# Optimization experiments

Hardware: AMD Instinct MI355X
Metric: run time of the kernel (lower is better)

Reference implementation:

```python
import jax, jax.numpy as jnp
import numpy as np
import math

N_LAYERS = 6
F = 512   # num_feature
H = 8     # num_head
DH = F // H
V = 32000 # vocab size
B = 64
S = 512   # == PositionalEncoding max_len
EPS = 1e-5


def _make_pe(max_len, d_model):
    position = np.arange(max_len, dtype=np.float32)[:, None]
    div_term = np.exp(np.arange(0, d_model, 2, dtype=np.float32) * (-math.log(10000.0) / d_model))
    pe = np.zeros((max_len, d_model), dtype=np.float32)
    pe[:, 0::2] = np.sin(position * div_term)
    pe[:, 1::2] = np.cos(position * div_term)
    return jnp.asarray(pe)


def setup_inputs() -> dict:
    key = jax.random.key(0)
    ks = jax.random.split(key, 16)
    w = lambda k, shape, s=0.02: (jax.random.normal(k, shape, dtype=jnp.float32) * s)
    inp = {
        "text": jax.random.randint(ks[0], (B, S), 0, V),
        "emb": jax.random.normal(ks[1], (V, F), dtype=jnp.float32) * 0.25,
        "pe": _make_pe(S, F),
        # per-layer params stacked on leading N axis
        "Wq": w(ks[2], (N_LAYERS, F, F)), "bq": jnp.zeros((N_LAYERS, F), jnp.float32),
        "Wk": w(ks[3], (N_LAYERS, F, F)), "bk": jnp.zeros((N_LAYERS, F), jnp.float32),
        "Wv": w(ks[4], (N_LAYERS, F, F)), "bv": jnp.zeros((N_LAYERS, F), jnp.float32),
        "g1": jnp.ones((N_LAYERS, F), jnp.float32), "beta1": jnp.zeros((N_LAYERS, F), jnp.float32),
        "Wf": w(ks[5], (N_LAYERS, F, F)), "bf": jnp.zeros((N_LAYERS, F), jnp.float32),
        "g2": jnp.ones((N_LAYERS, F), jnp.float32), "beta2": jnp.zeros((N_LAYERS, F), jnp.float32),
    }
    return inp


def _layernorm(x, g, b):
    m = jnp.mean(x, axis=-1, keepdims=True)
    v = jnp.mean(jnp.square(x - m), axis=-1, keepdims=True)
    return (x - m) * jax.lax.rsqrt(v + EPS) * g + b


def _encoder_layer(x, Wq, bq, Wk, bk, Wv, bv, g1, beta1, Wf, bf, g2, beta2):
    Bz, Sz, Fz = x.shape
    q = (x @ Wq + bq).reshape(Bz, Sz, H, DH)
    k = (x @ Wk + bk).reshape(Bz, Sz, H, DH)
    v = (x @ Wv + bv).reshape(Bz, Sz, H, DH)
    # FAITHFUL to source bug: attention over HEADS per token, no 1/sqrt(d) scaling.
    score = jnp.einsum('bshd,bsgd->bshg', q, k)          # [B,S,H,H]
    weight = jax.nn.softmax(score, axis=-1)
    attn = jnp.einsum('bshg,bsgd->bshd', weight, v).reshape(Bz, Sz, Fz)
    x = _layernorm(attn + x, g1, beta1)
    x = _layernorm((x @ Wf + bf) + x, g2, beta2)
    return x


def reference(text, emb, pe, Wq, bq, Wk, bk, Wv, bv, g1, beta1, Wf, bf, g2, beta2):
    x = emb[text] + pe[None, :text.shape[1], :]  # embedding + pos-enc (dropout = eval identity)
    for i in range(N_LAYERS):
        x = _encoder_layer(x, Wq[i], bq[i], Wk[i], bk[i], Wv[i], bv[i],
                           g1[i], beta1[i], Wf[i], bf[i], g2[i], beta2[i])
    return x
```

## Files before the change

kernel.cpp:

```cpp
#include <hip/hip_runtime.h>
#include <stdint.h>

typedef unsigned short u16;
using frag8 = __attribute__((ext_vector_type(8))) short;
using f32x4 = __attribute__((ext_vector_type(4))) float;

#define NTOK 32768
#define FDIM 512

__device__ __forceinline__ float bflo(uint32_t p){ union{uint32_t u; float f;} v; v.u = p<<16; return v.f; }
__device__ __forceinline__ float bfhi(uint32_t p){ union{uint32_t u; float f;} v; v.u = p & 0xffff0000u; return v.f; }
__device__ __forceinline__ float bf1(u16 x){ union{uint32_t u; float f;} v; v.u = ((uint32_t)x)<<16; return v.f; }
__device__ __forceinline__ u16 f2bf(float f){
  union{float f; uint32_t u;} v; v.f = f;
  uint32_t u = v.u;
  u += 0x7fffu + ((u>>16)&1u);
  return (u16)(u>>16);
}

__device__ __forceinline__ void async16(const void* g, void* l){
  __builtin_amdgcn_global_load_lds((const __attribute__((address_space(1))) uint32_t*)g,
                                   (__attribute__((address_space(3))) uint32_t*)l, 16, 0, 0);
}

__global__ __launch_bounds__(256) void embed_kernel(const int* __restrict__ text,
    const float* __restrict__ emb, const float* __restrict__ pe,
    u16* __restrict__ xb, const int tok0){
  const int gid = blockIdx.x*256 + threadIdx.x;
  const int base = gid*4;
  const int tl = base >> 9;
  const int f  = base & 511;
  const int tg = tl + tok0;
  const int s  = tg & 511;
  const int tok = text[tg];
  const float4 e4 = *(const float4*)(emb + (size_t)tok*FDIM + f);
  const float4 p4 = *(const float4*)(pe  + (size_t)s*FDIM + f);
  ushort4 ob;
  ob.x = f2bf(e4.x + p4.x);
  ob.y = f2bf(e4.y + p4.y);
  ob.z = f2bf(e4.z + p4.z);
  ob.w = f2bf(e4.w + p4.w);
  *(ushort4*)(xb + base) = ob;
}

__global__ __launch_bounds__(256) void transpose_w(const float* __restrict__ Wq,
    const float* __restrict__ Wk, const float* __restrict__ Wv, const float* __restrict__ Wf,
    u16* __restrict__ WT){
  const int gid = blockIdx.x*256 + threadIdx.x;
  const int n   = gid & 2047;
  const int k8  = (gid>>11) & 63;
  const int lay = gid >> 17;
  const float* src; int col;
  if      (n <  512){ src = Wq; col = n;      }
  else if (n < 1024){ src = Wk; col = n-512;  }
  else if (n < 1536){ src = Wv; col = n-1024; }
  else              { src = Wf; col = n-1536; }
  src += (size_t)lay*FDIM*FDIM;
  u16 vals[8] __attribute__((aligned(16)));
  #pragma unroll
  for (int i=0;i<8;i++) vals[i] = f2bf(src[(size_t)(k8*8+i)*FDIM + col]);
  *(int4*)(WT + ((size_t)lay*2048 + n)*FDIM + k8*8) = *(const int4*)vals;
}

template<int MODE>
__global__ __launch_bounds__(512, 2) void gemm256(
    const u16* __restrict__ A, const u16* __restrict__ BT,
    const float* __restrict__ b0, const float* __restrict__ b1, const float* __restrict__ b2,
    const u16* __restrict__ resid, u16* __restrict__ C, const int ldC, const int NB){
  __shared__ __attribute__((aligned(16))) short As[4*256*32];
  __shared__ __attribute__((aligned(16))) short Bs[4*256*32];
  const int nwg = gridDim.x;
  const int orig = blockIdx.x;
  const int wg = ((nwg & 7) == 0) ? ((orig & 7)*(nwg >> 3) + (orig >> 3)) : orig;
  const int nblk = wg % NB, mblk = wg / NB;
  const int m0 = mblk << 8, n0 = nblk << 8;
  const int tid = threadIdx.x;
  const int wid = tid >> 6, l = tid & 63;
  const int lm = l & 15, quad = l >> 4;

  const int srow = wid*16 + (l >> 2);
  const int sch  = (l & 3) ^ ((l >> 3) & 3);
  const char* Asrc0 = (const char*)A  + ((size_t)(m0 + srow))*1024 + sch*16;
  const char* Asrc1 = Asrc0 + 128*1024;
  const char* Bsrc0 = (const char*)BT + ((size_t)(n0 + srow))*1024 + sch*16;
  const char* Bsrc1 = Bsrc0 + 128*1024;
  char* ldsAw = (char*)As + wid*1024;
  char* ldsBw = (char*)Bs + wid*1024;

  f32x4 acc[8][4];
  #pragma unroll
  for (int i=0;i<8;i++)
    #pragma unroll
    for (int j=0;j<4;j++){ f32x4 z = {0.f,0.f,0.f,0.f}; acc[i][j] = z; }

  const int rsel = quad ^ ((lm >> 1) & 3);
  const int aB = ((wid>>2)*128 + lm)*32 + rsel*8;
  const int bB = ((wid&3)*64  + lm)*32 + rsel*8;

  #pragma unroll
  for (int kt=0; kt<3; kt++){
    async16(Asrc0 + kt*64, ldsAw + kt*16384);
    async16(Asrc1 + kt*64, ldsAw + kt*16384 + 8192);
    async16(Bsrc0 + kt*64, ldsBw + kt*16384);
    async16(Bsrc1 + kt*64, ldsBw + kt*16384 + 8192);
  }

  for (int t=0; t<16; ++t){
    if (t < 14)       asm volatile("s_waitcnt vmcnt(8)" ::: "memory");
    else if (t == 14) asm volatile("s_waitcnt vmcnt(4)" ::: "memory");
    else              asm volatile("s_waitcnt vmcnt(0)" ::: "memory");
    __builtin_amdgcn_s_barrier();
    asm volatile("" ::: "memory");
    const int slot = t & 3;
    const short* sA = As + slot*8192;
    const short* sB = Bs + slot*8192;
    frag8 af[4], bf[4], ag[4];
    #pragma unroll
    for (int mi=0; mi<4; mi++) af[mi] = *(const frag8*)(sA + aB + mi*512);
    #pragma unroll
    for (int nj=0; nj<4; nj++) bf[nj] = *(const frag8*)(sB + bB + nj*512);
    if (t < 13){
      const int s3 = (t+3) & 3, off = (t+3)*64;
      async16(Asrc0 + off, ldsAw + s3*16384);
      async16(Asrc1 + off, ldsAw + s3*16384 + 8192);
    }
    __builtin_amdgcn_s_setprio(1);
    #pragma unroll
    for (int mi=0; mi<4; mi++)
      #pragma unroll
      for (int nj=0; nj<4; nj++)
        acc[mi][nj] = __builtin_amdgcn_mfma_f32_16x16x32_bf16(af[mi], bf[nj], acc[mi][nj], 0,0,0);
    __builtin_amdgcn_s_setprio(0);
    #pragma unroll
    for (int mi=0; mi<4; mi++) ag[mi] = *(const frag8*)(sA + aB + 2048 + mi*512);
    if (t < 13){
      const int s3 = (t+3) & 3, off = (t+3)*64;
      async16(Bsrc0 + off, ldsBw + s3*16384);
      async16(Bsrc1 + off, ldsBw + s3*16384 + 8192);
    }
    __builtin_amdgcn_s_setprio(1);
    #pragma unroll
    for (int mi=0; mi<4; mi++)
      #pragma unroll
      for (int nj=0; nj<4; nj++)
        acc[4+mi][nj] = __builtin_amdgcn_mfma_f32_16x16x32_bf16(ag[mi], bf[nj], acc[4+mi][nj], 0,0,0);
    __builtin_amdgcn_s_setprio(0);
  }

  float bias[4]; int cols[4];
  #pragma unroll
  for (int nj=0;nj<4;nj++){
    const int c = n0 + (wid&3)*64 + nj*16 + lm;
    cols[nj] = c;
    if (MODE==0) bias[nj] = (c<512 ? b0[c] : (c<1024 ? b1[c-512] : b2[c-1024]));
    else         bias[nj] = b0[c];
  }
  #pragma unroll
  for (int mi=0; mi<8; mi++){
    const int rbase = m0 + (wid>>2)*128 + mi*16 + quad*4;
    #pragma unroll
    for (int r=0;r<4;r++){
      const size_t row = (size_t)(rbase + r);
      #pragma unroll
      for (int nj=0;nj<4;nj++){
        float v = acc[mi][nj][r] + bias[nj];
        if (MODE==1) v += bf1(resid[row*FDIM + cols[nj]]);
        C[row*(size_t)ldC + cols[nj]] = f2bf(v);
      }
    }
  }
}

__global__ __launch_bounds__(256) void attn_ln1(const u16* __restrict__ qkvb,
    const u16* __restrict__ xb, const float* __restrict__ gam, const float* __restrict__ bet,
    u16* __restrict__ y1b){
  __shared__ __attribute__((aligned(16))) u16 sQ[4][1536];
  __shared__ float sWt[4][64];
  const int tid = threadIdx.x, w = tid>>6, l = tid&63;
  const int t = blockIdx.x*4 + w;
  {
    const int4* src = (const int4*)(qkvb + (size_t)t*1536);
    int4* dst = (int4*)(&sQ[w][0]);
    #pragma unroll
    for (int i=0;i<3;i++) dst[i*64 + l] = src[i*64 + l];
  }
  __syncthreads();
  const int h = l>>3, g = l&7;
  const u16* qrow = &sQ[w][h*64];
  const u16* krow = &sQ[w][512 + g*64];
  float sc = 0.f;
  const int dstart = (l&31)*2;
  #pragma unroll
  for (int i=0;i<32;i++){
    const int d = (dstart + 2*i) & 63;
    const uint32_t qp = *(const uint32_t*)(qrow + d);
    const uint32_t kp = *(const uint32_t*)(krow + d);
    sc += bflo(qp)*bflo(kp) + bfhi(qp)*bfhi(kp);
  }
  float mx = sc;
  mx = fmaxf(mx, __shfl_xor(mx,1));
  mx = fmaxf(mx, __shfl_xor(mx,2));
  mx = fmaxf(mx, __shfl_xor(mx,4));
  const float e = __expf(sc - mx);
  float ssum = e;
  ssum += __shfl_xor(ssum,1);
  ssum += __shfl_xor(ssum,2);
  ssum += __shfl_xor(ssum,4);
  sWt[w][l] = e / ssum;
  __syncthreads();
  float wt[8];
  #pragma unroll
  for (int gg=0;gg<8;gg++) wt[gg] = sWt[w][h*8+gg];
  float att[8] = {0,0,0,0,0,0,0,0};
  const int d0 = (l&7)*8;
  #pragma unroll
  for (int gg=0;gg<8;gg++){
    const int4 vv = *(const int4*)(&sQ[w][1024 + gg*64 + d0]);
    const uint32_t* vp = (const uint32_t*)&vv;
    #pragma unroll
    for (int p=0;p<4;p++){
      att[2*p]   += wt[gg]*bflo(vp[p]);
      att[2*p+1] += wt[gg]*bfhi(vp[p]);
    }
  }
  const size_t rb = (size_t)t*FDIM + l*8;
  const int4 xv = *(const int4*)(xb + rb);
  const uint32_t* xp = (const uint32_t*)&xv;
  float y[8]; float s1=0.f, s2=0.f;
  #pragma unroll
  for (int p=0;p<4;p++){
    y[2*p]   = att[2*p]   + bflo(xp[p]);
    y[2*p+1] = att[2*p+1] + bfhi(xp[p]);
  }
  #pragma unroll
  for (int j=0;j<8;j++){ s1 += y[j]; s2 += y[j]*y[j]; }
  #pragma unroll
  for (int off=1; off<64; off<<=1){ s1 += __shfl_xor(s1,off); s2 += __shfl_xor(s2,off); }
  const float mean = s1*(1.f/512.f);
  const float var  = s2*(1.f/512.f) - mean*mean;
  const float rstd = rsqrtf(var + 1e-5f);
  const float4 g0 = *(const float4*)(gam + l*8);
  const float4 g1v = *(const float4*)(gam + l*8 + 4);
  const float4 b0v = *(const float4*)(bet + l*8);
  const float4 b1v = *(const float4*)(bet + l*8 + 4);
  float of[8];
  of[0]=(y[0]-mean)*rstd*g0.x + b0v.x;
  of[1]=(y[1]-mean)*rstd*g0.y + b0v.y;
  of[2]=(y[2]-mean)*rstd*g0.z + b0v.z;
  of[3]=(y[3]-mean)*rstd*g0.w + b0v.w;
  of[4]=(y[4]-mean)*rstd*g1v.x + b1v.x;
  of[5]=(y[5]-mean)*rstd*g1v.y + b1v.y;
  of[6]=(y[6]-mean)*rstd*g1v.z + b1v.z;
  of[7]=(y[7]-mean)*rstd*g1v.w + b1v.w;
  u16 ob[8] __attribute__((aligned(16)));
  #pragma unroll
  for (int j=0;j<8;j++) ob[j] = f2bf(of[j]);
  *(int4*)(y1b + rb) = *(const int4*)ob;
}

__global__ __launch_bounds__(256) void ln2_kernel(const u16* __restrict__ z,
    const float* __restrict__ gam, const float* __restrict__ bet,
    u16* __restrict__ xb, float* __restrict__ outp, const int final_){
  const int tid = threadIdx.x, w = tid>>6, l = tid&63;
  const int t = blockIdx.x*4 + w;
  const size_t rb = (size_t)t*FDIM + l*8;
  const int4 zv = *(const int4*)(z + rb);
  const uint32_t* zp = (const uint32_t*)&zv;
  float y[8];
  #pragma unroll
  for (int p=0;p<4;p++){ y[2*p]=bflo(zp[p]); y[2*p+1]=bfhi(zp[p]); }
  float s1=0.f, s2=0.f;
  #pragma unroll
  for (int j=0;j<8;j++){ s1+=y[j]; s2+=y[j]*y[j]; }
  #pragma unroll
  for (int off=1; off<64; off<<=1){ s1 += __shfl_xor(s1,off); s2 += __shfl_xor(s2,off); }
  const float mean = s1*(1.f/512.f);
  const float var  = s2*(1.f/512.f) - mean*mean;
  const float rstd = rsqrtf(var + 1e-5f);
  const float4 g0 = *(const float4*)(gam + l*8);
  const float4 g1v = *(const float4*)(gam + l*8 + 4);
  const float4 b0v = *(const float4*)(bet + l*8);
  const float4 b1v = *(const float4*)(bet + l*8 + 4);
  float of[8];
  of[0]=(y[0]-mean)*rstd*g0.x + b0v.x;
  of[1]=(y[1]-mean)*rstd*g0.y + b0v.y;
  of[2]=(y[2]-mean)*rstd*g0.z + b0v.z;
  of[3]=(y[3]-mean)*rstd*g0.w + b0v.w;
  of[4]=(y[4]-mean)*rstd*g1v.x + b1v.x;
  of[5]=(y[5]-mean)*rstd*g1v.y + b1v.y;
  of[6]=(y[6]-mean)*rstd*g1v.z + b1v.z;
  of[7]=(y[7]-mean)*rstd*g1v.w + b1v.w;
  if (final_){
    float4 o0; o0.x=of[0]; o0.y=of[1]; o0.z=of[2]; o0.w=of[3];
    float4 o1; o1.x=of[4]; o1.y=of[5]; o1.z=of[6]; o1.w=of[7];
    *(float4*)(outp + rb) = o0;
    *(float4*)(outp + rb + 4) = o1;
  } else {
    u16 ob[8] __attribute__((aligned(16)));
    #pragma unroll
    for (int j=0;j<8;j++) ob[j] = f2bf(of[j]);
    *(int4*)(xb + rb) = *(const int4*)ob;
  }
}

extern "C" void kernel_launch(void* const* d_in, const int* in_sizes, int n_in,
                              void* d_out, int out_size, void* d_ws, size_t ws_size,
                              hipStream_t stream){
  const int*   text = (const int*)d_in[0];
  const float* emb = (const float*)d_in[1];
  const float* pe  = (const float*)d_in[2];
  const float* Wq  = (const float*)d_in[3];
  const float* bq  = (const float*)d_in[4];
  const float* Wk  = (const float*)d_in[5];
  const float* bk  = (const float*)d_in[6];
  const float* Wv  = (const float*)d_in[7];
  const float* bv  = (const float*)d_in[8];
  const float* g1  = (const float*)d_in[9];
  const float* be1 = (const float*)d_in[10];
  const float* Wf  = (const float*)d_in[11];
  const float* bf_ = (const float*)d_in[12];
  const float* g2  = (const float*)d_in[13];
  const float* be2 = (const float*)d_in[14];
  float* outp = (float*)d_out;

  const size_t wtB = (size_t)6*2048*512*2;
  int T = NTOK;
  while (T > 2048 && wtB + (size_t)T*5120 > ws_size) T >>= 1;

  char* ws = (char*)d_ws;
  u16*   WT  = (u16*)ws;
  char*  act = ws + wtB;
  u16*   xb  = (u16*)act;
  u16*   y1b = (u16*)(act + (size_t)T*1024);
  u16*   qkv = (u16*)(act + (size_t)T*2048);
  u16*   zb  = qkv;

  hipLaunchKernelGGL(transpose_w, dim3(3072), dim3(256), 0, stream, Wq, Wk, Wv, Wf, WT);

  const int chunks = NTOK / T;
  for (int c = 0; c < chunks; c++){
    const int tok0 = c*T;
    hipLaunchKernelGGL(embed_kernel, dim3(T/2), dim3(256), 0, stream, text, emb, pe, xb, tok0);
    for (int lay=0; lay<6; lay++){
      const u16* WTl = WT + (size_t)lay*2048*FDIM;
      hipLaunchKernelGGL((gemm256<0>), dim3((T/256)*6), dim3(512), 0, stream,
          xb, WTl, bq + lay*FDIM, bk + lay*FDIM, bv + lay*FDIM, (const u16*)nullptr, qkv, 1536, 6);
      hipLaunchKernelGGL(attn_ln1, dim3(T/4), dim3(256), 0, stream,
          qkv, xb, g1 + lay*FDIM, be1 + lay*FDIM, y1b);
      hipLaunchKernelGGL((gemm256<1>), dim3((T/256)*2), dim3(512), 0, stream,
          y1b, WTl + (size_t)1536*FDIM, bf_ + lay*FDIM, (const float*)nullptr, (const float*)nullptr,
          y1b, zb, 512, 2);
      hipLaunchKernelGGL(ln2_kernel, dim3(T/4), dim3(256), 0, stream,
          zb, g2 + lay*FDIM, be2 + lay*FDIM, xb, outp + (size_t)tok0*FDIM, (lay==5)?1:0);
    }
  }
}
```

Measured before the change: 969.0 us.

## Software-pipeline LDS fragment loads across K-tiles in GEMM main loop

Restructures the GEMM K-loop so the A and B fragments for the next tile are read from LDS while the second half of the current tile's MFMAs runs. B fragments are double-buffered in registers. The wait and barrier move mid-tile, with an extra barrier at the end of each step to protect slot reuse. The goal is to hide LDS read latency behind MFMA work, at the cost of more registers and an extra barrier per step.

```diff
diff --git a/kernel.cpp b/kernel.cpp
--- a/kernel.cpp
+++ b/kernel.cpp
@@ -104,48 +104,67 @@
     async16(Bsrc0 + kt*64, ldsBw + kt*16384);
     async16(Bsrc1 + kt*64, ldsBw + kt*16384 + 8192);
   }
-
-  for (int t=0; t<16; ++t){
-    if (t < 14)       asm volatile("s_waitcnt vmcnt(8)" ::: "memory");
-    else if (t == 14) asm volatile("s_waitcnt vmcnt(4)" ::: "memory");
-    else              asm volatile("s_waitcnt vmcnt(0)" ::: "memory");
-    __builtin_amdgcn_s_barrier();
-    asm volatile("" ::: "memory");
-    const int slot = t & 3;
-    const short* sA = As + slot*8192;
-    const short* sB = Bs + slot*8192;
-    frag8 af[4], bf[4], ag[4];
-    #pragma unroll
-    for (int mi=0; mi<4; mi++) af[mi] = *(const frag8*)(sA + aB + mi*512);
-    #pragma unroll
-    for (int nj=0; nj<4; nj++) bf[nj] = *(const frag8*)(sB + bB + nj*512);
-    if (t < 13){
-      const int s3 = (t+3) & 3, off = (t+3)*64;
-      async16(Asrc0 + off, ldsAw + s3*16384);
-      async16(Asrc1 + off, ldsAw + s3*16384 + 8192);
-    }
-    __builtin_amdgcn_s_setprio(1);
-    #pragma unroll
-    for (int mi=0; mi<4; mi++)
-      #pragma unroll
-      for (int nj=0; nj<4; nj++)
-        acc[mi][nj] = __builtin_amdgcn_mfma_f32_16x16x32_bf16(af[mi], bf[nj], acc[mi][nj], 0,0,0);
-    __builtin_amdgcn_s_setprio(0);
-    #pragma unroll
-    for (int mi=0; mi<4; mi++) ag[mi] = *(const frag8*)(sA + aB + 2048 + mi*512);
-    if (t < 13){
-      const int s3 = (t+3) & 3, off = (t+3)*64;
-      async16(Bsrc0 + off, ldsBw + s3*16384);
-      async16(Bsrc1 + off, ldsBw + s3*16384 + 8192);
-    }
-    __builtin_amdgcn_s_setprio(1);
-    #pragma unroll
-    for (int mi=0; mi<4; mi++)
-      #pragma unroll
-      for (int nj=0; nj<4; nj++)
-        acc[4+mi][nj] = __builtin_amdgcn_mfma_f32_16x16x32_bf16(ag[mi], bf[nj], acc[4+mi][nj], 0,0,0);
-    __builtin_amdgcn_s_setprio(0);
-  }
+  frag8 aC[4], aN[4], bE[4], bO[4];
+  asm volatile("s_waitcnt vmcnt(8)" ::: "memory");
+  __builtin_amdgcn_s_barrier();
+  #pragma unroll
+  for (int x=0;x<4;x++){
+    aC[x] = *(const frag8*)(As + aB + x*512);
+    bE[x] = *(const frag8*)(Bs + bB + x*512);
+  }
+
+#define MFMA16(AF, BF, RO) \
+  __builtin_amdgcn_s_setprio(1); \
+  _Pragma("unroll") \
+  for (int mi_=0; mi_<4; mi_++) \
+    _Pragma("unroll") \
+    for (int nj_=0; nj_<4; nj_++) \
+      acc[(RO)+mi_][nj_] = __builtin_amdgcn_mfma_f32_16x16x32_bf16(AF[mi_], BF[nj_], acc[(RO)+mi_][nj_], 0,0,0); \
+  __builtin_amdgcn_s_setprio(0);
+
+#define TILE_BODY(T_, BU, BL, DOSTAGE, VMC) { \
+  const short* sA_ = As + ((T_)&3)*8192; \
+  if (DOSTAGE){ \
+    const int s3_ = ((T_)+3)&3; const int off_ = ((T_)+3)*64; \
+    async16(Asrc0 + off_, ldsAw + s3_*16384); \
+    async16(Asrc1 + off_, ldsAw + s3_*16384 + 8192); \
+  } \
+  _Pragma("unroll") \
+  for (int x_=0;x_<4;x_++) aN[x_] = *(const frag8*)(sA_ + aB + 2048 + x_*512); \
+  MFMA16(aC, BU, 0) \
+  if (DOSTAGE){ \
+    const int s3_ = ((T_)+3)&3; const int off_ = ((T_)+3)*64; \
+    async16(Bsrc0 + off_, ldsBw + s3_*16384); \
+    async16(Bsrc1 + off_, ldsBw + s3_*16384 + 8192); \
+  } \
+  asm volatile("s_waitcnt vmcnt(" #VMC ")" ::: "memory"); \
+  __builtin_amdgcn_s_barrier(); \
+  { const short* sA2_ = As + (((T_)+1)&3)*8192; \
+    const short* sB2_ = Bs + (((T_)+1)&3)*8192; \
+    _Pragma("unroll") \
+    for (int x_=0;x_<4;x_++){ \
+      aC[x_] = *(const frag8*)(sA2_ + aB + x_*512); \
+      BL[x_] = *(const frag8*)(sB2_ + bB + x_*512); } } \
+  MFMA16(aN, BU, 4) \
+  __builtin_amdgcn_s_barrier(); \
+}
+
+  for (int tp=0; tp<6; ++tp){
+    TILE_BODY(2*tp,   bE, bO, 1, 8)
+    TILE_BODY(2*tp+1, bO, bE, 1, 8)
+  }
+  TILE_BODY(12, bE, bO, 1, 8)
+  TILE_BODY(13, bO, bE, 0, 4)
+  TILE_BODY(14, bE, bO, 0, 0)
+  {
+    const short* sA_ = As + 3*8192;
+    #pragma unroll
+    for (int x=0;x<4;x++) aN[x] = *(const frag8*)(sA_ + aB + 2048 + x*512);
+    MFMA16(aC, bO, 0)
+    MFMA16(aN, bO, 4)
+  }
+#undef TILE_BODY
+#undef MFMA16
 
   float bias[4]; int cols[4];
   #pragma unroll
```

Result: faster. 916.3 us (-5.4%).

## Shrink GEMM tiles to 128x128 with 4 waves and 3-stage LDS pipeline

Applied to the files above, without the earlier changes.

Replaces the 256x256-tile, 8-wave GEMM, which used a 4-slot LDS ring, with a 128x128-tile, 4-wave kernel that uses a 3-slot ring and a fully unrolled K loop. The grids grow by 4x, which improves load balance and occupancy (3 blocks per CU, less LDS per block). The cost is more global and L2 traffic per FLOP, since each tile reuses less data, and a shallower prefetch depth.

```diff
diff --git a/kernel.cpp b/kernel.cpp
--- a/kernel.cpp
+++ b/kernel.cpp
@@ -63,17 +63,17 @@
 }
 
 template<int MODE>
-__global__ __launch_bounds__(512, 2) void gemm256(
+__global__ __launch_bounds__(256, 3) void gemm128(
     const u16* __restrict__ A, const u16* __restrict__ BT,
     const float* __restrict__ b0, const float* __restrict__ b1, const float* __restrict__ b2,
     const u16* __restrict__ resid, u16* __restrict__ C, const int ldC, const int NB){
-  __shared__ __attribute__((aligned(16))) short As[4*256*32];
-  __shared__ __attribute__((aligned(16))) short Bs[4*256*32];
+  __shared__ __attribute__((aligned(16))) short As[3*128*32];
+  __shared__ __attribute__((aligned(16))) short Bs[3*128*32];
   const int nwg = gridDim.x;
   const int orig = blockIdx.x;
   const int wg = ((nwg & 7) == 0) ? ((orig & 7)*(nwg >> 3) + (orig >> 3)) : orig;
   const int nblk = wg % NB, mblk = wg / NB;
-  const int m0 = mblk << 8, n0 = nblk << 8;
+  const int m0 = mblk << 7, n0 = nblk << 7;
   const int tid = threadIdx.x;
   const int wid = tid >> 6, l = tid & 63;
   const int lm = l & 15, quad = l >> 4;
@@ -81,83 +81,72 @@
   const int srow = wid*16 + (l >> 2);
   const int sch  = (l & 3) ^ ((l >> 3) & 3);
   const char* Asrc0 = (const char*)A  + ((size_t)(m0 + srow))*1024 + sch*16;
-  const char* Asrc1 = Asrc0 + 128*1024;
+  const char* Asrc1 = Asrc0 + 64*1024;
   const char* Bsrc0 = (const char*)BT + ((size_t)(n0 + srow))*1024 + sch*16;
-  const char* Bsrc1 = Bsrc0 + 128*1024;
+  const char* Bsrc1 = Bsrc0 + 64*1024;
   char* ldsAw = (char*)As + wid*1024;
   char* ldsBw = (char*)Bs + wid*1024;
 
-  f32x4 acc[8][4];
-  #pragma unroll
-  for (int i=0;i<8;i++)
+  f32x4 acc[4][4];
+  #pragma unroll
+  for (int i=0;i<4;i++)
     #pragma unroll
     for (int j=0;j<4;j++){ f32x4 z = {0.f,0.f,0.f,0.f}; acc[i][j] = z; }
 
   const int rsel = quad ^ ((lm >> 1) & 3);
-  const int aB = ((wid>>2)*128 + lm)*32 + rsel*8;
-  const int bB = ((wid&3)*64  + lm)*32 + rsel*8;
-
-  #pragma unroll
-  for (int kt=0; kt<3; kt++){
-    async16(Asrc0 + kt*64, ldsAw + kt*16384);
-    async16(Asrc1 + kt*64, ldsAw + kt*16384 + 8192);
-    async16(Bsrc0 + kt*64, ldsBw + kt*16384);
-    async16(Bsrc1 + kt*64, ldsBw + kt*16384 + 8192);
-  }
-
-  for (int t=0; t<16; ++t){
-    if (t < 14)       asm volatile("s_waitcnt vmcnt(8)" ::: "memory");
-    else if (t == 14) asm volatile("s_waitcnt vmcnt(4)" ::: "memory");
-    else              asm volatile("s_waitcnt vmcnt(0)" ::: "memory");
-    __builtin_amdgcn_s_barrier();
-    asm volatile("" ::: "memory");
-    const int slot = t & 3;
-    const short* sA = As + slot*8192;
-    const short* sB = Bs + slot*8192;
-    frag8 af[4], bf[4], ag[4];
-    #pragma unroll
-    for (int mi=0; mi<4; mi++) af[mi] = *(const frag8*)(sA + aB + mi*512);
-    #pragma unroll
-    for (int nj=0; nj<4; nj++) bf[nj] = *(const frag8*)(sB + bB + nj*512);
-    if (t < 13){
-      const int s3 = (t+3) & 3, off = (t+3)*64;
-      async16(Asrc0 + off, ldsAw + s3*16384);
-      async16(Asrc1 + off, ldsAw + s3*16384 + 8192);
-    }
-    __builtin_amdgcn_s_setprio(1);
-    #pragma unroll
-    for (int mi=0; mi<4; mi++)
-      #pragma unroll
-      for (int nj=0; nj<4; nj++)
-        acc[mi][nj] = __builtin_amdgcn_mfma_f32_16x16x32_bf16(af[mi], bf[nj], acc[mi][nj], 0,0,0);
-    __builtin_amdgcn_s_setprio(0);
-    #pragma unroll
-    for (int mi=0; mi<4; mi++) ag[mi] = *(const frag8*)(sA + aB + 2048 + mi*512);
-    if (t < 13){
-      const int s3 = (t+3) & 3, off = (t+3)*64;
-      async16(Bsrc0 + off, ldsBw + s3*16384);
-      async16(Bsrc1 + off, ldsBw + s3*16384 + 8192);
-    }
-    __builtin_amdgcn_s_setprio(1);
-    #pragma unroll
-    for (int mi=0; mi<4; mi++)
-      #pragma unroll
-      for (int nj=0; nj<4; nj++)
-        acc[4+mi][nj] = __builtin_amdgcn_mfma_f32_16x16x32_bf16(ag[mi], bf[nj], acc[4+mi][nj], 0,0,0);
-    __builtin_amdgcn_s_setprio(0);
-  }
+  const int aB = ((wid>>1)*64 + lm)*32 + rsel*8;
+  const int bB = ((wid&1)*64  + lm)*32 + rsel*8;
+
+  #pragma unroll
+  for (int kt=0; kt<2; kt++){
+    async16(Asrc0 + kt*64, ldsAw + kt*8192);
+    async16(Asrc1 + kt*64, ldsAw + kt*8192 + 4096);
+    async16(Bsrc0 + kt*64, ldsBw + kt*8192);
+    async16(Bsrc1 + kt*64, ldsBw + kt*8192 + 4096);
+  }
+
+#define TILE(T_, DOSTAGE, VMC) { \
+    asm volatile("s_waitcnt vmcnt(" #VMC ")" ::: "memory"); \
+    __builtin_amdgcn_s_barrier(); \
+    asm volatile("" ::: "memory"); \
+    if (DOSTAGE){ const int s_ = ((T_)+2)%3; const int off_ = ((T_)+2)*64; \
+      async16(Asrc0 + off_, ldsAw + s_*8192); \
+      async16(Asrc1 + off_, ldsAw + s_*8192 + 4096); } \
+    const short* sA_ = As + ((T_)%3)*4096; \
+    const short* sB_ = Bs + ((T_)%3)*4096; \
+    frag8 af_[4], bf_[4]; \
+    _Pragma("unroll") \
+    for (int x_=0;x_<4;x_++) af_[x_] = *(const frag8*)(sA_ + aB + x_*512); \
+    _Pragma("unroll") \
+    for (int x_=0;x_<4;x_++) bf_[x_] = *(const frag8*)(sB_ + bB + x_*512); \
+    if (DOSTAGE){ const int s_ = ((T_)+2)%3; const int off_ = ((T_)+2)*64; \
+      async16(Bsrc0 + off_, ldsBw + s_*8192); \
+      async16(Bsrc1 + off_, ldsBw + s_*8192 + 4096); } \
+    __builtin_amdgcn_s_setprio(1); \
+    _Pragma("unroll") \
+    for (int mi_=0;mi_<4;mi_++) \
+      _Pragma("unroll") \
+      for (int nj_=0;nj_<4;nj_++) \
+        acc[mi_][nj_] = __builtin_amdgcn_mfma_f32_16x16x32_bf16(af_[mi_], bf_[nj_], acc[mi_][nj_], 0,0,0); \
+    __builtin_amdgcn_s_setprio(0); }
+
+  TILE(0,1,4)  TILE(1,1,4)  TILE(2,1,4)  TILE(3,1,4)
+  TILE(4,1,4)  TILE(5,1,4)  TILE(6,1,4)  TILE(7,1,4)
+  TILE(8,1,4)  TILE(9,1,4)  TILE(10,1,4) TILE(11,1,4)
+  TILE(12,1,4) TILE(13,1,4) TILE(14,0,4) TILE(15,0,0)
+#undef TILE
 
   float bias[4]; int cols[4];
   #pragma unroll
   for (int nj=0;nj<4;nj++){
-    const int c = n0 + (wid&3)*64 + nj*16 + lm;
+    const int c = n0 + (wid&1)*64 + nj*16 + lm;
     cols[nj] = c;
     if (MODE==0) bias[nj] = (c<512 ? b0[c] : (c<1024 ? b1[c-512] : b2[c-1024]));
     else         bias[nj] = b0[c];
   }
   #pragma unroll
-  for (int mi=0; mi<8; mi++){
-    const int rbase = m0 + (wid>>2)*128 + mi*16 + quad*4;
+  for (int mi=0; mi<4; mi++){
+    const int rbase = m0 + (wid>>1)*64 + mi*16 + quad*4;
     #pragma unroll
     for (int r=0;r<4;r++){
       const size_t row = (size_t)(rbase + r);
@@ -343,13 +332,13 @@
     hipLaunchKernelGGL(embed_kernel, dim3(T/2), dim3(256), 0, stream, text, emb, pe, xb, tok0);
     for (int lay=0; lay<6; lay++){
       const u16* WTl = WT + (size_t)lay*2048*FDIM;
-      hipLaunchKernelGGL((gemm256<0>), dim3((T/256)*6), dim3(512), 0, stream,
-          xb, WTl, bq + lay*FDIM, bk + lay*FDIM, bv + lay*FDIM, (const u16*)nullptr, qkv, 1536, 6);
+      hipLaunchKernelGGL((gemm128<0>), dim3((T/128)*12), dim3(256), 0, stream,
+          xb, WTl, bq + lay*FDIM, bk + lay*FDIM, bv + lay*FDIM, (const u16*)nullptr, qkv, 1536, 12);
       hipLaunchKernelGGL(attn_ln1, dim3(T/4), dim3(256), 0, stream,
           qkv, xb, g1 + lay*FDIM, be1 + lay*FDIM, y1b);
-      hipLaunchKernelGGL((gemm256<1>), dim3((T/256)*2), dim3(512), 0, stream,
+      hipLaunchKernelGGL((gemm128<1>), dim3((T/128)*4), dim3(256), 0, stream,
           y1b, WTl + (size_t)1536*FDIM, bf_ + lay*FDIM, (const float*)nullptr, (const float*)nullptr,
-          y1b, zb, 512, 2);
+          y1b, zb, 512, 4);
       hipLaunchKernelGGL(ln2_kernel, dim3(T/4), dim3(256), 0, stream,
           zb, g2 + lay*FDIM, be2 + lay*FDIM, xb, outp + (size_t)tok0*FDIM, (lay==5)?1:0);
     }
```

Result: no change. 968.7 us (-0.0%).

## Fuse attention+LN1, feedforward GEMM, and LN2 into one kernel per layer

Applied to the files above, without the earlier changes.

Replaces three kernels (attn_ln1, the FF gemm256<1>, ln2_kernel) with one attn_ff_fused kernel. Each 64-token block computes head attention and LN1 into LDS, runs the 512x512 FF GEMM from LDS with double-buffered async weight loads, then applies bias, residual and LN2 in-register with a cross-wave reduction. This removes the global round trips for y1 and z and two launches per layer. In exchange the FF GEMM uses smaller 64-row tiles and reloads the full weight matrix per block. It also rests on a large LDS footprint and a serial per-wave attention loop before the GEMM starts.

```diff
diff --git a/kernel.cpp b/kernel.cpp
--- a/kernel.cpp
+++ b/kernel.cpp
@@ -114,11 +114,11 @@
     const int slot = t & 3;
     const short* sA = As + slot*8192;
     const short* sB = Bs + slot*8192;
-    frag8 af[4], bf[4], ag[4];
+    frag8 af[4], bfrg[4], ag[4];
     #pragma unroll
     for (int mi=0; mi<4; mi++) af[mi] = *(const frag8*)(sA + aB + mi*512);
     #pragma unroll
-    for (int nj=0; nj<4; nj++) bf[nj] = *(const frag8*)(sB + bB + nj*512);
+    for (int nj=0; nj<4; nj++) bfrg[nj] = *(const frag8*)(sB + bB + nj*512);
     if (t < 13){
       const int s3 = (t+3) & 3, off = (t+3)*64;
       async16(Asrc0 + off, ldsAw + s3*16384);
@@ -129,7 +129,7 @@
     for (int mi=0; mi<4; mi++)
       #pragma unroll
       for (int nj=0; nj<4; nj++)
-        acc[mi][nj] = __builtin_amdgcn_mfma_f32_16x16x32_bf16(af[mi], bf[nj], acc[mi][nj], 0,0,0);
+        acc[mi][nj] = __builtin_amdgcn_mfma_f32_16x16x32_bf16(af[mi], bfrg[nj], acc[mi][nj], 0,0,0);
     __builtin_amdgcn_s_setprio(0);
     #pragma unroll
     for (int mi=0; mi<4; mi++) ag[mi] = *(const frag8*)(sA + aB + 2048 + mi*512);
@@ -143,7 +143,7 @@
     for (int mi=0; mi<4; mi++)
       #pragma unroll
       for (int nj=0; nj<4; nj++)
-        acc[4+mi][nj] = __builtin_amdgcn_mfma_f32_16x16x32_bf16(ag[mi], bf[nj], acc[4+mi][nj], 0,0,0);
+        acc[4+mi][nj] = __builtin_amdgcn_mfma_f32_16x16x32_bf16(ag[mi], bfrg[nj], acc[4+mi][nj], 0,0,0);
     __builtin_amdgcn_s_setprio(0);
   }
 
@@ -171,135 +171,222 @@
   }
 }
 
-__global__ __launch_bounds__(256) void attn_ln1(const u16* __restrict__ qkvb,
-    const u16* __restrict__ xb, const float* __restrict__ gam, const float* __restrict__ bet,
-    u16* __restrict__ y1b){
-  __shared__ __attribute__((aligned(16))) u16 sQ[4][1536];
-  __shared__ float sWt[4][64];
-  const int tid = threadIdx.x, w = tid>>6, l = tid&63;
-  const int t = blockIdx.x*4 + w;
+__global__ __launch_bounds__(512, 2) void attn_ff_fused(
+    const u16* __restrict__ qkvb, u16* __restrict__ xb,
+    const u16* __restrict__ WTf,
+    const float* __restrict__ g1, const float* __restrict__ be1,
+    const float* __restrict__ bfv,
+    const float* __restrict__ g2, const float* __restrict__ be2,
+    float* __restrict__ outp, const int final_){
+  __shared__ __attribute__((aligned(16))) short y1S[64*512];
+  __shared__ __attribute__((aligned(16))) short Bs[2*512*32];
+  const int m0 = blockIdx.x * 64;
+  const int tid = threadIdx.x;
+  const int wid = tid>>6, l = tid&63;
+  const int lm = l&15, quad = l>>4;
+  const int wm = wid>>2, wn = wid&3;
+
+  const int sch = (l&3) ^ ((l>>3)&3);
+  const u16* bsrc = WTf + (size_t)(wid*16 + (l>>2))*512 + sch*8;
+  char* ldsBw = (char*)Bs + wid*1024;
+
+#define STAGEB(TT_, S_) { \
+    _Pragma("unroll") \
+    for (int r_=0;r_<4;r_++) \
+      async16(bsrc + (TT_)*32 + r_*65536, ldsBw + (S_)*32768 + r_*8192); }
+
+  STAGEB(0, 0)
+
   {
-    const int4* src = (const int4*)(qkvb + (size_t)t*1536);
-    int4* dst = (int4*)(&sQ[w][0]);
-    #pragma unroll
-    for (int i=0;i<3;i++) dst[i*64 + l] = src[i*64 + l];
+    char* scr = (char*)Bs + 32768 + wid*4096;
+    u16* sq = (u16*)scr;
+    float* swt = (float*)(scr + 3072);
+    const float4 ga0 = *(const float4*)(g1 + l*8);
+    const float4 ga1 = *(const float4*)(g1 + l*8 + 4);
+    const float4 bb0 = *(const float4*)(be1 + l*8);
+    const float4 bb1 = *(const float4*)(be1 + l*8 + 4);
+    for (int tk=0; tk<8; tk++){
+      const int t = m0 + wid*8 + tk;
+      {
+        const int4* src = (const int4*)(qkvb + (size_t)t*1536);
+        int4* dst = (int4*)sq;
+        #pragma unroll
+        for (int i=0;i<3;i++) dst[i*64 + l] = src[i*64 + l];
+      }
+      const int h = l>>3, g = l&7;
+      const u16* qrow = sq + h*64;
+      const u16* krow = sq + 512 + g*64;
+      float sc = 0.f;
+      const int dstart = (l&31)*2;
+      #pragma unroll
+      for (int i=0;i<32;i++){
+        const int d = (dstart + 2*i) & 63;
+        const uint32_t qp = *(const uint32_t*)(qrow + d);
+        const uint32_t kp = *(const uint32_t*)(krow + d);
+        sc += bflo(qp)*bflo(kp) + bfhi(qp)*bfhi(kp);
+      }
+      float mx = sc;
+      mx = fmaxf(mx, __shfl_xor(mx,1));
+      mx = fmaxf(mx, __shfl_xor(mx,2));
+      mx = fmaxf(mx, __shfl_xor(mx,4));
+      const float e = __expf(sc - mx);
+      float ssum = e;
+      ssum += __shfl_xor(ssum,1);
+      ssum += __shfl_xor(ssum,2);
+      ssum += __shfl_xor(ssum,4);
+      swt[l] = e / ssum;
+      float wt[8];
+      #pragma unroll
+      for (int gg=0;gg<8;gg++) wt[gg] = swt[h*8+gg];
+      float att[8] = {0,0,0,0,0,0,0,0};
+      const int d0 = (l&7)*8;
+      #pragma unroll
+      for (int gg=0;gg<8;gg++){
+        const int4 vv = *(const int4*)(sq + 1024 + gg*64 + d0);
+        const uint32_t* vp = (const uint32_t*)&vv;
+        #pragma unroll
+        for (int p=0;p<4;p++){
+          att[2*p]   += wt[gg]*bflo(vp[p]);
+          att[2*p+1] += wt[gg]*bfhi(vp[p]);
+        }
+      }
+      const size_t rb = (size_t)t*FDIM + l*8;
+      const int4 xv = *(const int4*)(xb + rb);
+      const uint32_t* xp = (const uint32_t*)&xv;
+      float y[8]; float s1=0.f, s2=0.f;
+      #pragma unroll
+      for (int p=0;p<4;p++){
+        y[2*p]   = att[2*p]   + bflo(xp[p]);
+        y[2*p+1] = att[2*p+1] + bfhi(xp[p]);
+      }
+      #pragma unroll
+      for (int j=0;j<8;j++){ s1 += y[j]; s2 += y[j]*y[j]; }
+      #pragma unroll
+      for (int off=1; off<64; off<<=1){ s1 += __shfl_xor(s1,off); s2 += __shfl_xor(s2,off); }
+      const float mean = s1*(1.f/512.f);
+      const float var  = s2*(1.f/512.f) - mean*mean;
+      const float rstd = rsqrtf(var + 1e-5f);
+      float of[8];
+      of[0]=(y[0]-mean)*rstd*ga0.x + bb0.x;
+      of[1]=(y[1]-mean)*rstd*ga0.y + bb0.y;
+      of[2]=(y[2]-mean)*rstd*ga0.z + bb0.z;
+      of[3]=(y[3]-mean)*rstd*ga0.w + bb0.w;
+      of[4]=(y[4]-mean)*rstd*ga1.x + bb1.x;
+      of[5]=(y[5]-mean)*rstd*ga1.y + bb1.y;
+      of[6]=(y[6]-mean)*rstd*ga1.z + bb1.z;
+      of[7]=(y[7]-mean)*rstd*ga1.w + bb1.w;
+      u16 ob[8] __attribute__((aligned(16)));
+      #pragma unroll
+      for (int j=0;j<8;j++) ob[j] = f2bf(of[j]);
+      const int tl = wid*8 + tk;
+      const int fx = ((tl>>1)&3) | (((tl>>3)&1)<<2);
+      *(int4*)((char*)y1S + tl*1024 + ((l ^ fx)<<4)) = *(const int4*)ob;
+    }
   }
   __syncthreads();
-  const int h = l>>3, g = l&7;
-  const u16* qrow = &sQ[w][h*64];
-  const u16* krow = &sQ[w][512 + g*64];
-  float sc = 0.f;
-  const int dstart = (l&31)*2;
-  #pragma unroll
-  for (int i=0;i<32;i++){
-    const int d = (dstart + 2*i) & 63;
-    const uint32_t qp = *(const uint32_t*)(qrow + d);
-    const uint32_t kp = *(const uint32_t*)(krow + d);
-    sc += bflo(qp)*bflo(kp) + bfhi(qp)*bfhi(kp);
-  }
-  float mx = sc;
-  mx = fmaxf(mx, __shfl_xor(mx,1));
-  mx = fmaxf(mx, __shfl_xor(mx,2));
-  mx = fmaxf(mx, __shfl_xor(mx,4));
-  const float e = __expf(sc - mx);
-  float ssum = e;
-  ssum += __shfl_xor(ssum,1);
-  ssum += __shfl_xor(ssum,2);
-  ssum += __shfl_xor(ssum,4);
-  sWt[w][l] = e / ssum;
+
+  f32x4 acc[2][8];
+  #pragma unroll
+  for (int i=0;i<2;i++)
+    #pragma unroll
+    for (int j=0;j<8;j++){ f32x4 z = {0.f,0.f,0.f,0.f}; acc[i][j] = z; }
+  const int axor = ((lm>>1)&3) | (((lm>>3)&1)<<2);
+  const int aBase = (wm*32 + lm)*512;
+  const int bOff = (wn*128 + lm)*32 + (quad ^ ((lm>>1)&3))*8;
+
+#define FTILE2(T_, DOSTAGE) { \
+    asm volatile("s_waitcnt vmcnt(0)" ::: "memory"); \
+    __builtin_amdgcn_s_barrier(); \
+    asm volatile("" ::: "memory"); \
+    if (DOSTAGE){ STAGEB((T_)+1, ((T_)+1)&1) } \
+    const short* sB_ = Bs + ((T_)&1)*16384; \
+    frag8 af_[2], bf_[8]; \
+    _Pragma("unroll") \
+    for (int mi_=0;mi_<2;mi_++) \
+      af_[mi_] = *(const frag8*)(y1S + aBase + mi_*8192 + (((((T_)*4)+quad)^axor)<<3)); \
+    _Pragma("unroll") \
+    for (int nj_=0;nj_<8;nj_++) bf_[nj_] = *(const frag8*)(sB_ + bOff + nj_*512); \
+    __builtin_amdgcn_s_setprio(1); \
+    _Pragma("unroll") \
+    for (int mi_=0;mi_<2;mi_++) \
+      _Pragma("unroll") \
+      for (int nj_=0;nj_<8;nj_++) \
+        acc[mi_][nj_] = __builtin_amdgcn_mfma_f32_16x16x32_bf16(af_[mi_], bf_[nj_], acc[mi_][nj_], 0,0,0); \
+    __builtin_amdgcn_s_setprio(0); }
+
+  FTILE2(0,1)  FTILE2(1,1)  FTILE2(2,1)  FTILE2(3,1)
+  FTILE2(4,1)  FTILE2(5,1)  FTILE2(6,1)  FTILE2(7,1)
+  FTILE2(8,1)  FTILE2(9,1)  FTILE2(10,1) FTILE2(11,1)
+  FTILE2(12,1) FTILE2(13,1) FTILE2(14,1) FTILE2(15,0)
+#undef FTILE2
+#undef STAGEB
+
   __syncthreads();
-  float wt[8];
-  #pragma unroll
-  for (int gg=0;gg<8;gg++) wt[gg] = sWt[w][h*8+gg];
-  float att[8] = {0,0,0,0,0,0,0,0};
-  const int d0 = (l&7)*8;
-  #pragma unroll
-  for (int gg=0;gg<8;gg++){
-    const int4 vv = *(const int4*)(&sQ[w][1024 + gg*64 + d0]);
-    const uint32_t* vp = (const uint32_t*)&vv;
-    #pragma unroll
-    for (int p=0;p<4;p++){
-      att[2*p]   += wt[gg]*bflo(vp[p]);
-      att[2*p+1] += wt[gg]*bfhi(vp[p]);
-    }
-  }
-  const size_t rb = (size_t)t*FDIM + l*8;
-  const int4 xv = *(const int4*)(xb + rb);
-  const uint32_t* xp = (const uint32_t*)&xv;
-  float y[8]; float s1=0.f, s2=0.f;
-  #pragma unroll
-  for (int p=0;p<4;p++){
-    y[2*p]   = att[2*p]   + bflo(xp[p]);
-    y[2*p+1] = att[2*p+1] + bfhi(xp[p]);
-  }
-  #pragma unroll
-  for (int j=0;j<8;j++){ s1 += y[j]; s2 += y[j]*y[j]; }
-  #pragma unroll
-  for (int off=1; off<64; off<<=1){ s1 += __shfl_xor(s1,off); s2 += __shfl_xor(s2,off); }
-  const float mean = s1*(1.f/512.f);
-  const float var  = s2*(1.f/512.f) - mean*mean;
-  const float rstd = rsqrtf(var + 1e-5f);
-  const float4 g0 = *(const float4*)(gam + l*8);
-  const float4 g1v = *(const float4*)(gam + l*8 + 4);
-  const float4 b0v = *(const float4*)(bet + l*8);
-  const float4 b1v = *(const float4*)(bet + l*8 + 4);
-  float of[8];
-  of[0]=(y[0]-mean)*rstd*g0.x + b0v.x;
-  of[1]=(y[1]-mean)*rstd*g0.y + b0v.y;
-  of[2]=(y[2]-mean)*rstd*g0.z + b0v.z;
-  of[3]=(y[3]-mean)*rstd*g0.w + b0v.w;
-  of[4]=(y[4]-mean)*rstd*g1v.x + b1v.x;
-  of[5]=(y[5]-mean)*rstd*g1v.y + b1v.y;
-  of[6]=(y[6]-mean)*rstd*g1v.z + b1v.z;
-  of[7]=(y[7]-mean)*rstd*g1v.w + b1v.w;
-  u16 ob[8] __attribute__((aligned(16)));
-  #pragma unroll
-  for (int j=0;j<8;j++) ob[j] = f2bf(of[j]);
-  *(int4*)(y1b + rb) = *(const int4*)ob;
-}
-
-__global__ __launch_bounds__(256) void ln2_kernel(const u16* __restrict__ z,
-    const float* __restrict__ gam, const float* __restrict__ bet,
-    u16* __restrict__ xb, float* __restrict__ outp, const int final_){
-  const int tid = threadIdx.x, w = tid>>6, l = tid&63;
-  const int t = blockIdx.x*4 + w;
-  const size_t rb = (size_t)t*FDIM + l*8;
-  const int4 zv = *(const int4*)(z + rb);
-  const uint32_t* zp = (const uint32_t*)&zv;
-  float y[8];
-  #pragma unroll
-  for (int p=0;p<4;p++){ y[2*p]=bflo(zp[p]); y[2*p+1]=bfhi(zp[p]); }
-  float s1=0.f, s2=0.f;
-  #pragma unroll
-  for (int j=0;j<8;j++){ s1+=y[j]; s2+=y[j]*y[j]; }
-  #pragma unroll
-  for (int off=1; off<64; off<<=1){ s1 += __shfl_xor(s1,off); s2 += __shfl_xor(s2,off); }
-  const float mean = s1*(1.f/512.f);
-  const float var  = s2*(1.f/512.f) - mean*mean;
-  const float rstd = rsqrtf(var + 1e-5f);
-  const float4 g0 = *(const float4*)(gam + l*8);
-  const float4 g1v = *(const float4*)(gam + l*8 + 4);
-  const float4 b0v = *(const float4*)(bet + l*8);
-  const float4 b1v = *(const float4*)(bet + l*8 + 4);
-  float of[8];
-  of[0]=(y[0]-mean)*rstd*g0.x + b0v.x;
-  of[1]=(y[1]-mean)*rstd*g0.y + b0v.y;
-  of[2]=(y[2]-mean)*rstd*g0.z + b0v.z;
-  of[3]=(y[3]-mean)*rstd*g0.w + b0v.w;
-  of[4]=(y[4]-mean)*rstd*g1v.x + b1v.x;
-  of[5]=(y[5]-mean)*rstd*g1v.y + b1v.y;
-  of[6]=(y[6]-mean)*rstd*g1v.z + b1v.z;
-  of[7]=(y[7]-mean)*rstd*g1v.w + b1v.w;
-  if (final_){
-    float4 o0; o0.x=of[0]; o0.y=of[1]; o0.z=of[2]; o0.w=of[3];
-    float4 o1; o1.x=of[4]; o1.y=of[5]; o1.z=of[6]; o1.w=of[7];
-    *(float4*)(outp + rb) = o0;
-    *(float4*)(outp + rb + 4) = o1;
-  } else {
-    u16 ob[8] __attribute__((aligned(16)));
-    #pragma unroll
-    for (int j=0;j<8;j++) ob[j] = f2bf(of[j]);
-    *(int4*)(xb + rb) = *(const int4*)ob;
+  float* ln2S = (float*)Bs;
+  int cols[8]; float bia[8], gg2[8], be2v[8];
+  #pragma unroll
+  for (int nj=0;nj<8;nj++){
+    const int c = wn*128 + nj*16 + lm;
+    cols[nj] = c; bia[nj] = bfv[c]; gg2[nj] = g2[c]; be2v[nj] = be2[c];
+  }
+  #pragma unroll
+  for (int mi=0;mi<2;mi++){
+    #pragma unroll
+    for (int r=0;r<4;r++){
+      const int row_l = wm*32 + mi*16 + quad*4 + r;
+      const int frow = ((row_l>>1)&3) | (((row_l>>3)&1)<<2);
+      #pragma unroll
+      for (int nj=0;nj<8;nj++){
+        const int c = cols[nj];
+        const float resid = bf1(y1S[row_l*512 + (((c>>3)^frow)<<3) + (c&7)]);
+        acc[mi][nj][r] += bia[nj] + resid;
+      }
+    }
+  }
+  #pragma unroll
+  for (int mi=0;mi<2;mi++){
+    #pragma unroll
+    for (int r=0;r<4;r++){
+      const int row_l = wm*32 + mi*16 + quad*4 + r;
+      float s1 = 0.f, s2 = 0.f;
+      #pragma unroll
+      for (int nj=0;nj<8;nj++){ const float v = acc[mi][nj][r]; s1 += v; s2 += v*v; }
+      s1 += __shfl_xor(s1,1); s2 += __shfl_xor(s2,1);
+      s1 += __shfl_xor(s1,2); s2 += __shfl_xor(s2,2);
+      s1 += __shfl_xor(s1,4); s2 += __shfl_xor(s2,4);
+      s1 += __shfl_xor(s1,8); s2 += __shfl_xor(s2,8);
+      if (lm == 0){
+        ln2S[row_l*8 + wn*2]     = s1;
+        ln2S[row_l*8 + wn*2 + 1] = s2;
+      }
+    }
+  }
+  __syncthreads();
+  #pragma unroll
+  for (int mi=0;mi<2;mi++){
+    #pragma unroll
+    for (int r=0;r<4;r++){
+      const int row_l = wm*32 + mi*16 + quad*4 + r;
+      const float s1t = ln2S[row_l*8] + ln2S[row_l*8+2] + ln2S[row_l*8+4] + ln2S[row_l*8+6];
+      const float s2t = ln2S[row_l*8+1] + ln2S[row_l*8+3] + ln2S[row_l*8+5] + ln2S[row_l*8+7];
+      const float mean = s1t*(1.f/512.f);
+      const float var  = s2t*(1.f/512.f) - mean*mean;
+      const float rstd = rsqrtf(var + 1e-5f);
+      const size_t rg = (size_t)(m0 + row_l)*FDIM;
+      if (final_){
+        #pragma unroll
+        for (int nj=0;nj<8;nj++){
+          const float of = (acc[mi][nj][r]-mean)*rstd*gg2[nj] + be2v[nj];
+          outp[rg + cols[nj]] = of;
+        }
+      } else {
+        #pragma unroll
+        for (int nj=0;nj<8;nj++){
+          const float of = (acc[mi][nj][r]-mean)*rstd*gg2[nj] + be2v[nj];
+          xb[rg + cols[nj]] = f2bf(of);
+        }
+      }
+    }
   }
 }
 
@@ -325,15 +412,13 @@
 
   const size_t wtB = (size_t)6*2048*512*2;
   int T = NTOK;
-  while (T > 2048 && wtB + (size_t)T*5120 > ws_size) T >>= 1;
+  while (T > 2048 && wtB + (size_t)T*4096 > ws_size) T >>= 1;
 
   char* ws = (char*)d_ws;
   u16*   WT  = (u16*)ws;
   char*  act = ws + wtB;
   u16*   xb  = (u16*)act;
-  u16*   y1b = (u16*)(act + (size_t)T*1024);
-  u16*   qkv = (u16*)(act + (size_t)T*2048);
-  u16*   zb  = qkv;
+  u16*   qkv = (u16*)(act + (size_t)T*1024);
 
   hipLaunchKernelGGL(transpose_w, dim3(3072), dim3(256), 0, stream, Wq, Wk, Wv, Wf, WT);
 
@@ -345,13 +430,11 @@
       const u16* WTl = WT + (size_t)lay*2048*FDIM;
       hipLaunchKernelGGL((gemm256<0>), dim3((T/256)*6), dim3(512), 0, stream,
           xb, WTl, bq + lay*FDIM, bk + lay*FDIM, bv + lay*FDIM, (const u16*)nullptr, qkv, 1536, 6);
-      hipLaunchKernelGGL(attn_ln1, dim3(T/4), dim3(256), 0, stream,
-          qkv, xb, g1 + lay*FDIM, be1 + lay*FDIM, y1b);
-      hipLaunchKernelGGL((gemm256<1>), dim3((T/256)*2), dim3(512), 0, stream,
-          y1b, WTl + (size_t)1536*FDIM, bf_ + lay*FDIM, (const float*)nullptr, (const float*)nullptr,
-          y1b, zb, 512, 2);
-      hipLaunchKernelGGL(ln2_kernel, dim3(T/4), dim3(256), 0, stream,
-          zb, g2 + lay*FDIM, be2 + lay*FDIM, xb, outp + (size_t)tok0*FDIM, (lay==5)?1:0);
-    }
-  }
-}
+      hipLaunchKernelGGL(attn_ff_fused, dim3(T/64), dim3(512), 0, stream,
+          qkv, xb, WTl + (size_t)1536*FDIM,
+          g1 + lay*FDIM, be1 + lay*FDIM, bf_ + lay*FDIM,
+          g2 + lay*FDIM, be2 + lay*FDIM,
+          outp + (size_t)tok0*FDIM, (lay==5)?1:0);
+    }
+  }
+}
```

New measurement: 1.092 ms. 1.13x slower.
